# Kernel tuning notes

Hardware: AMD Instinct MI355X
Metric: run time of the kernel (lower is better)

## Reference

```python
import jax, jax.numpy as jnp
import numpy as np

B, N, D = 32, 2048, 128
HALF = D // 2
DT = 0.01  # interval = [0.0, 0.01], euler solver -> single step of size 0.01


def setup_inputs() -> dict:
    key = jax.random.key(0)
    ks = jax.random.split(key, 10)
    x = jax.random.normal(ks[0], (B, N, D), dtype=jnp.float32)
    hz = jax.random.normal(ks[1], (B, N, D), dtype=jnp.float32)
    # row-normalized random adjacency so adj @ h stays O(1) (avoids tanh saturation)
    adj = jax.random.uniform(ks[2], (N, N), dtype=jnp.float32) / N
    W1 = jax.random.normal(ks[3], (D, D), dtype=jnp.float32) * 0.05
    W2 = jax.random.normal(ks[4], (D, D), dtype=jnp.float32) * 0.05
    Wa = jax.random.normal(ks[5], (2 * D, 2 * D), dtype=jnp.float32) * 0.05
    ba = jnp.zeros((2 * D,), dtype=jnp.float32)
    Wb = jax.random.normal(ks[6], (2 * D, D), dtype=jnp.float32) * 0.05
    bb = jnp.zeros((D,), dtype=jnp.float32)
    # nn.Parameter init is zeros in torch; randomize in [0,0.1] for a nontrivial baseline
    eps = jax.random.uniform(ks[7], (B, N, HALF), dtype=jnp.float32) * 0.1
    return {"x": x, "hz": hz, "adj": adj, "W1": W1, "W2": W2,
            "Wa": Wa, "ba": ba, "Wb": Wb, "bb": bb, "eps": eps}


def reference(x, hz, adj, W1, W2, Wa, ba, Wb, bb, eps):
    # MLP gating: Linear(2D,2D) -> ReLU -> Linear(2D,D) -> Tanh
    u = jnp.concatenate([x, hz], axis=-1)            # [B,N,2D]
    h = jnp.tanh(jax.nn.relu(u @ Wa + ba) @ Wb + bb)  # [B,N,D]

    def gnn_func(h, W):
        # f(t, h) = tanh(A @ h @ W)  (graph diffusion ODE func)
        return jnp.tanh(jnp.einsum('nm,bmd->bnd', adj, h) @ W)

    def euler_step(h, W):
        # odeint(euler, t=[0, 0.01]): one step y1 = y0 + dt * f(0, y0)
        return h + DT * gnn_func(h, W)

    eps_c = jnp.clip(eps, 0.0, 0.1)
    for _ in range(2):
        h_f = euler_step(h, W1)[..., :HALF]                      # [B,N,D/2]
        h = jnp.concatenate([h_f, h[..., HALF:]], axis=-1)       # [B,N,D]
        h_s = eps_c * euler_step(h, W2)[..., HALF:]              # [B,N,D/2]
        h = jnp.concatenate([h_f, h_s], axis=-1)                 # [B,N,D]
    return h
```

## Files before the change

### kernel.cpp

```cpp
#include <hip/hip_runtime.h>


typedef unsigned short u16;
typedef unsigned int   u32;
typedef unsigned long long u64;
typedef __attribute__((ext_vector_type(8))) short bf8;
typedef __attribute__((ext_vector_type(4))) float f4;

#define AS1 __attribute__((address_space(1)))
#define AS3 __attribute__((address_space(3)))

__device__ __forceinline__ void gl_lds16(const void* g, void* l) {
  __builtin_amdgcn_global_load_lds((const AS1 u32*)g, (AS3 u32*)l, 16, 0, 0);
}
__device__ __forceinline__ float bf2f(u16 v) {
  u32 u = ((u32)v) << 16; return __builtin_bit_cast(float, u);
}
__device__ __forceinline__ u16 f2bf(float f) {
  u32 u = __builtin_bit_cast(u32, f);
  return (u16)((u + 0x7fffu + ((u >> 16) & 1u)) >> 16);
}
__device__ __forceinline__ float ldf(const void* p, size_t i, u32 isf32) {
  return isf32 ? ((const float*)p)[i] : bf2f(((const u16*)p)[i]);
}

__device__ __forceinline__ void stage128x32(const u16* grow0, int stride, u16* lds,
                                            int wave, int lane) {
  int r0 = wave * 16 + (lane >> 2);
  int c0 = (lane & 3) * 8;
  gl_lds16(grow0 + (size_t)r0 * stride + c0, lds + wave * 512);
  gl_lds16(grow0 + (size_t)(64 + r0) * stride + c0, lds + 2048 + wave * 512);
}

__global__ void detect_dtype(const u16* __restrict__ x_raw, u32* __restrict__ flag) {
  __shared__ int s;
  int tid = threadIdx.x;
  if (tid == 0) s = 0;
  __syncthreads();
  int huge = 0;
#pragma unroll
  for (int j = 0; j < 16; ++j) {
    u16 v = x_raw[tid * 16 + j];
    u32 e = (v >> 7) & 0xFF;
    if (e >= 0xC0) huge = 1;
  }
  if (huge) atomicOr(&s, 1);
  __syncthreads();
  if (tid == 0) flag[0] = (u32)s;
}

__global__ void cvt_bf16(const void* __restrict__ in, u16* __restrict__ out,
                         long in_off, int n, const u32* __restrict__ flag) {
  u32 isf32 = flag[0];
  int gid = blockIdx.x * 256 + threadIdx.x;
  long i = in_off + (long)gid * 4;
  if (gid * 4 >= n) return;
  u16 o0, o1, o2, o3;
  if (isf32) {
    f4 v = *(const f4*)&((const float*)in)[i];
    o0 = f2bf(v[0]); o1 = f2bf(v[1]); o2 = f2bf(v[2]); o3 = f2bf(v[3]);
  } else {
    u64 v = *(const u64*)&((const u16*)in)[i];
    o0 = (u16)v; o1 = (u16)(v >> 16); o2 = (u16)(v >> 32); o3 = (u16)(v >> 48);
  }
  u64 pk = (u64)o0 | ((u64)o1 << 16) | ((u64)o2 << 32) | ((u64)o3 << 48);
  *(u64*)&out[(size_t)gid * 4] = pk;
}

__global__ void prep_weights(const void* __restrict__ Wa, const void* __restrict__ Wb,
                             const void* __restrict__ W1, const void* __restrict__ W2,
                             u16* __restrict__ WaT, u16* __restrict__ WbT,
                             u16* __restrict__ W1T, u16* __restrict__ W2T,
                             const u32* __restrict__ flag) {
  u32 isf32 = flag[0];
  int i = blockIdx.x * 256 + threadIdx.x;
  if (i < 65536) {
    int o = i >> 8, k = i & 255; WaT[o * 256 + k] = f2bf(ldf(Wa, (size_t)k * 256 + o, isf32));
  } else if (i < 98304) {
    int j = i - 65536; int o = j >> 8, k = j & 255;
    WbT[o * 256 + k] = f2bf(ldf(Wb, (size_t)k * 128 + o, isf32));
  } else if (i < 106496) {
    int j = i - 98304; int jj = j >> 7, k = j & 127;
    W1T[jj * 128 + k] = f2bf(ldf(W1, (size_t)k * 128 + jj, isf32));
  } else {
    int j = i - 106496; int jj = j >> 7, k = j & 127;
    W2T[jj * 128 + k] = f2bf(ldf(W2, (size_t)k * 128 + 64 + jj, isf32));
  }
}

__global__ __launch_bounds__(256, 2) void mlp_fused(const void* __restrict__ x,
                                                    const void* __restrict__ hz,
                                                    const u16* __restrict__ WaT,
                                                    const void* __restrict__ ba,
                                                    const u16* __restrict__ WbT,
                                                    const void* __restrict__ bb,
                                                    u16* __restrict__ hT,
                                                    const u32* __restrict__ flag) {
  __shared__ __align__(16) u16 Z[64 * 264];
  __shared__ __align__(16) u16 lA[64 * 32];
  __shared__ __align__(16) u16 lB[256 * 32];
  u32 isf32 = flag[0];
  int tid = threadIdx.x, lane = tid & 63, wave = tid >> 6;
  int col = lane & 15, quad = lane >> 4;
  int r0 = blockIdx.x * 64;

  f4 acc[4][4] = {};
  for (int kk = 0; kk < 8; ++kk) {
    int k0 = kk * 32;
    const void* src = (kk < 4) ? x : hz;
    int csrc = (kk < 4) ? k0 : (k0 - 128);
    __syncthreads();
    {
      int row = tid >> 2, c0 = (tid & 3) * 8;
      size_t g = (size_t)(r0 + row) * 128 + csrc + c0;
      uint4 pk;
      if (isf32) {
        f4 v0 = *(const f4*)&((const float*)src)[g];
        f4 v1 = *(const f4*)&((const float*)src)[g + 4];
        pk.x = (u32)f2bf(v0[0]) | ((u32)f2bf(v0[1]) << 16);
        pk.y = (u32)f2bf(v0[2]) | ((u32)f2bf(v0[3]) << 16);
        pk.z = (u32)f2bf(v1[0]) | ((u32)f2bf(v1[1]) << 16);
        pk.w = (u32)f2bf(v1[2]) | ((u32)f2bf(v1[3]) << 16);
      } else {
        pk = *(const uint4*)&((const u16*)src)[g];
      }
      *(uint4*)&lA[row * 32 + c0] = pk;
    }
    stage128x32(WaT + k0, 256, lB, wave, lane);
    stage128x32(WaT + (size_t)128 * 256 + k0, 256, lB + 4096, wave, lane);
    __syncthreads();
    bf8 af[4], bfr[4];
#pragma unroll
    for (int mi = 0; mi < 4; ++mi) af[mi] = *(const bf8*)&lA[(mi * 16 + col) * 32 + quad * 8];
#pragma unroll
    for (int nj = 0; nj < 4; ++nj) bfr[nj] = *(const bf8*)&lB[(wave * 64 + nj * 16 + col) * 32 + quad * 8];
#pragma unroll
    for (int mi = 0; mi < 4; ++mi)
#pragma unroll
      for (int nj = 0; nj < 4; ++nj)
        acc[mi][nj] = __builtin_amdgcn_mfma_f32_16x16x32_bf16(af[mi], bfr[nj], acc[mi][nj], 0, 0, 0);
  }
#pragma unroll
  for (int mi = 0; mi < 4; ++mi)
#pragma unroll
    for (int nj = 0; nj < 4; ++nj) {
      int o = wave * 64 + nj * 16 + col;
      float bav = ldf(ba, o, isf32);
      int rl = mi * 16 + quad * 4;
#pragma unroll
      for (int r = 0; r < 4; ++r)
        Z[(rl + r) * 264 + o] = f2bf(fmaxf(acc[mi][nj][r] + bav, 0.f));
    }
  __syncthreads();

  f4 acc2[4][2] = {};
  for (int kk = 0; kk < 8; ++kk) {
    int k0 = kk * 32;
    if (kk) __syncthreads();
    stage128x32(WbT + k0, 256, lB, wave, lane);
    __syncthreads();
    bf8 az[4], bw[2];
#pragma unroll
    for (int mi = 0; mi < 4; ++mi) az[mi] = *(const bf8*)&Z[(mi * 16 + col) * 264 + k0 + quad * 8];
#pragma unroll
    for (int nj = 0; nj < 2; ++nj) bw[nj] = *(const bf8*)&lB[(wave * 32 + nj * 16 + col) * 32 + quad * 8];
#pragma unroll
    for (int mi = 0; mi < 4; ++mi)
#pragma unroll
      for (int nj = 0; nj < 2; ++nj)
        acc2[mi][nj] = __builtin_amdgcn_mfma_f32_16x16x32_bf16(az[mi], bw[nj], acc2[mi][nj], 0, 0, 0);
  }
#pragma unroll
  for (int mi = 0; mi < 4; ++mi)
#pragma unroll
    for (int nj = 0; nj < 2; ++nj) {
      int d = wave * 32 + nj * 16 + col;
      float bbv = ldf(bb, d, isf32);
      int rabs = r0 + mi * 16 + quad * 4;
      int b = rabs >> 11, n = rabs & 2047;
      u16 p[4];
#pragma unroll
      for (int r = 0; r < 4; ++r) p[r] = f2bf(tanhf(acc2[mi][nj][r] + bbv));
      u64 pk = (u64)p[0] | ((u64)p[1] << 16) | ((u64)p[2] << 32) | ((u64)p[3] << 48);
      *(u64*)&hT[(size_t)(b * 128 + d) * 2048 + n] = pk;
    }
}

__global__ __launch_bounds__(256, 2) void fused_step(const u16* __restrict__ hin,
                                                     const u16* __restrict__ adjb,
                                                     const u16* __restrict__ WT,
                                                     const void* __restrict__ eps,
                                                     u16* __restrict__ hout,
                                                     int half, const u32* __restrict__ flag) {
  __shared__ __align__(16) u16 lA[2][128 * 32];
  __shared__ __align__(16) u16 lB[2][128 * 32];
  __shared__ __align__(16) u16 gT[128 * 136];
  u32 isf32 = flag[0];
  int tid = threadIdx.x, lane = tid & 63, wave = tid >> 6;
  int wm = wave >> 1, wn = wave & 1, col = lane & 15, quad = lane >> 4;
  int b = blockIdx.y;
  int n0 = blockIdx.x * 128;

  const u16* Arow = hin + (size_t)(b * 128) * 2048;
  const u16* Brow = adjb + (size_t)n0 * 2048;

  stage128x32(Arow, 2048, lA[0], wave, lane);
  stage128x32(Brow, 2048, lB[0], wave, lane);
  __syncthreads();

  f4 acc[4][4] = {};
  for (int kk = 0; kk < 64; ++kk) {
    int cur = kk & 1;
    if (kk < 63) {
      stage128x32(Arow + (kk + 1) * 32, 2048, lA[cur ^ 1], wave, lane);
      stage128x32(Brow + (kk + 1) * 32, 2048, lB[cur ^ 1], wave, lane);
    }
    bf8 af[4], bfr[4];
#pragma unroll
    for (int mi = 0; mi < 4; ++mi) af[mi] = *(const bf8*)&lA[cur][(wm * 64 + mi * 16 + col) * 32 + quad * 8];
#pragma unroll
    for (int nj = 0; nj < 4; ++nj) bfr[nj] = *(const bf8*)&lB[cur][(wn * 64 + nj * 16 + col) * 32 + quad * 8];
#pragma unroll
    for (int mi = 0; mi < 4; ++mi)
#pragma unroll
      for (int nj = 0; nj < 4; ++nj)
        acc[mi][nj] = __builtin_amdgcn_mfma_f32_16x16x32_bf16(af[mi], bfr[nj], acc[mi][nj], 0, 0, 0);
    __syncthreads();
  }
#pragma unroll
  for (int mi = 0; mi < 4; ++mi)
#pragma unroll
    for (int nj = 0; nj < 4; ++nj) {
      int d0 = wm * 64 + mi * 16 + quad * 4;
      int nl = wn * 64 + nj * 16 + col;
      u32 lo = (u32)f2bf(acc[mi][nj][0]) | ((u32)f2bf(acc[mi][nj][1]) << 16);
      u32 hi = (u32)f2bf(acc[mi][nj][2]) | ((u32)f2bf(acc[mi][nj][3]) << 16);
      *(u64*)&gT[nl * 136 + d0] = (u64)lo | ((u64)hi << 32);
    }
  __syncthreads();

  f4 acc2[4][2] = {};
#pragma unroll
  for (int k2 = 0; k2 < 4; ++k2) {
    bf8 aw[4], bg[2];
#pragma unroll
    for (int mi = 0; mi < 4; ++mi)
      aw[mi] = *(const bf8*)&WT[(size_t)(mi * 16 + col) * 128 + k2 * 32 + quad * 8];
#pragma unroll
    for (int nj = 0; nj < 2; ++nj)
      bg[nj] = *(const bf8*)&gT[(wave * 32 + nj * 16 + col) * 136 + k2 * 32 + quad * 8];
#pragma unroll
    for (int mi = 0; mi < 4; ++mi)
#pragma unroll
      for (int nj = 0; nj < 2; ++nj)
        acc2[mi][nj] = __builtin_amdgcn_mfma_f32_16x16x32_bf16(aw[mi], bg[nj], acc2[mi][nj], 0, 0, 0);
  }

  bool has_eps = (eps != nullptr);
#pragma unroll
  for (int mi = 0; mi < 4; ++mi)
#pragma unroll
    for (int nj = 0; nj < 2; ++nj) {
      int j0 = mi * 16 + quad * 4;
      int nl = wave * 32 + nj * 16 + col;
      int n = n0 + nl;
      float ev[4];
      if (has_eps) {
        size_t eoff = ((size_t)b * 2048 + n) * 64 + j0;
        if (isf32) {
          f4 e = *(const f4*)&((const float*)eps)[eoff];
          ev[0] = e[0]; ev[1] = e[1]; ev[2] = e[2]; ev[3] = e[3];
        } else {
          u64 e = *(const u64*)&((const u16*)eps)[eoff];
          ev[0] = bf2f((u16)e); ev[1] = bf2f((u16)(e >> 16));
          ev[2] = bf2f((u16)(e >> 32)); ev[3] = bf2f((u16)(e >> 48));
        }
      }
#pragma unroll
      for (int r = 0; r < 4; ++r) {
        int j = j0 + r;
        size_t idx = (size_t)(b * 128 + half * 64 + j) * 2048 + n;
        float hold = bf2f(hin[idx]);
        float nh = hold + 0.01f * tanhf(acc2[mi][nj][r]);
        if (has_eps) {
          float e = fminf(fmaxf(ev[r], 0.f), 0.1f);
          nh = e * nh;
        }
        hout[idx] = f2bf(nh);
      }
    }

  {
    int oh = (1 - half) * 64;
    const u16* src = hin + (size_t)(b * 128 + oh) * 2048 + n0;
    u16* dst = hout + (size_t)(b * 128 + oh) * 2048 + n0;
#pragma unroll
    for (int i = 0; i < 4; ++i) {
      int idx = i * 256 + tid;
      int rr = idx >> 4;
      int cc = (idx & 15) * 8;
      *(uint4*)&dst[(size_t)rr * 2048 + cc] = *(const uint4*)&src[(size_t)rr * 2048 + cc];
    }
  }
}

__global__ void untranspose(const u16* __restrict__ hT, void* __restrict__ out,
                            const u32* __restrict__ flag) {
  __shared__ __align__(16) u16 t[64][65];
  u32 isf32 = flag[0];
  int b = blockIdx.z, d0 = blockIdx.y * 64, n0 = blockIdx.x * 64;
  int tid = threadIdx.x;
#pragma unroll
  for (int i = 0; i < 16; ++i) {
    int idx = tid + i * 256;
    int r = idx >> 6, c = idx & 63;
    t[r][c] = hT[(size_t)(b * 128 + d0 + r) * 2048 + n0 + c];
  }
  __syncthreads();
#pragma unroll
  for (int i = 0; i < 16; ++i) {
    int idx = tid + i * 256;
    int r = idx >> 6, c = idx & 63;
    size_t o = (size_t)(b * 2048 + n0 + r) * 128 + d0 + c;
    if (isf32) ((float*)out)[o] = bf2f(t[c][r]);
    else       ((u16*)out)[o] = t[c][r];
  }
}

extern "C" void kernel_launch(void* const* d_in, const int* in_sizes, int n_in,
                              void* d_out, int out_size, void* d_ws, size_t ws_size,
                              hipStream_t stream) {
  const void* x   = d_in[0];
  const void* hz  = d_in[1];
  const void* adj = d_in[2];
  const void* W1  = d_in[3];
  const void* W2  = d_in[4];
  const void* Wa  = d_in[5];
  const void* ba  = d_in[6];
  const void* Wb  = d_in[7];
  const void* bb  = d_in[8];
  const void* eps = d_in[9];

  char* ws = (char*)d_ws;
  u16* hA   = (u16*)(ws);
  u16* adjb = (u16*)(ws + (17ull << 20));
  u16* WaT  = (u16*)(ws + (26ull << 20));
  u16* WbT  = WaT + 256 * 256;
  u16* W1T  = WbT + 128 * 256;
  u16* W2T  = W1T + 64 * 128;
  u32* flag = (u32*)(W2T + 64 * 128);
  u16* hB   = (u16*)d_out;

  detect_dtype<<<dim3(1), dim3(256), 0, stream>>>((const u16*)x, flag);
  prep_weights<<<dim3(448), dim3(256), 0, stream>>>(Wa, Wb, W1, W2, WaT, WbT, W1T, W2T, flag);
  cvt_bf16<<<dim3(4096), dim3(256), 0, stream>>>(adj, adjb, 0, 4194304, flag);
  mlp_fused<<<dim3(1024), dim3(256), 0, stream>>>(x, hz, WaT, ba, WbT, bb, hA, flag);
  fused_step<<<dim3(16, 32), dim3(256), 0, stream>>>(hA, adjb, W1T, nullptr, hB, 0, flag);
  fused_step<<<dim3(16, 32), dim3(256), 0, stream>>>(hB, adjb, W2T, eps, hA, 1, flag);
  fused_step<<<dim3(16, 32), dim3(256), 0, stream>>>(hA, adjb, W1T, nullptr, hB, 0, flag);
  fused_step<<<dim3(16, 32), dim3(256), 0, stream>>>(hB, adjb, W2T, eps, hA, 1, flag);
  untranspose<<<dim3(32, 2, 32), dim3(256), 0, stream>>>(hA, d_out, flag);
}
```

Baseline: 412.1 us.

## Reassociate adj@(h@W) so graph GEMM contracts only 64 needed columns

Uses associativity to compute h@W (only the 64 output columns each step needs) before the adjacency product. The projection is fused into the epilogue of the previous kernel (MLP or prior step), which writes a transposed hW buffer. The big N×N GEMM then has a 64-wide rather than 128-wide operand, halving its MFMA work and A-operand traffic. In exchange, the main loop now stages 4 K-slices per barrier without double buffering, and extra bf16 rounding of the intermediate hW alters numerics.

```diff
diff --git a/kernel.cpp b/kernel.cpp
--- a/kernel.cpp
+++ b/kernel.cpp
@@ -30,6 +30,11 @@
   int c0 = (lane & 3) * 8;
   gl_lds16(grow0 + (size_t)r0 * stride + c0, lds + wave * 512);
   gl_lds16(grow0 + (size_t)(64 + r0) * stride + c0, lds + 2048 + wave * 512);
+}
+__device__ __forceinline__ void stage64x32(const u16* grow0, int stride, u16* lds,
+                                           int wave, int lane) {
+  gl_lds16(grow0 + (size_t)(wave * 16 + (lane >> 2)) * stride + (lane & 3) * 8,
+           lds + wave * 512);
 }
 
 __global__ void detect_dtype(const u16* __restrict__ x_raw, u32* __restrict__ flag) {
@@ -94,15 +99,20 @@
                                                     const void* __restrict__ ba,
                                                     const u16* __restrict__ WbT,
                                                     const void* __restrict__ bb,
+                                                    const u16* __restrict__ W1T,
                                                     u16* __restrict__ hT,
+                                                    u16* __restrict__ hW,
                                                     const u32* __restrict__ flag) {
   __shared__ __align__(16) u16 Z[64 * 264];
-  __shared__ __align__(16) u16 lA[64 * 32];
-  __shared__ __align__(16) u16 lB[256 * 32];
+  __shared__ __align__(16) u16 pool[10240];
+  u16* lA = pool;
+  u16* lB = pool + 2048;
+  u16* hN = pool;
   u32 isf32 = flag[0];
   int tid = threadIdx.x, lane = tid & 63, wave = tid >> 6;
   int col = lane & 15, quad = lane >> 4;
   int r0 = blockIdx.x * 64;
+  int b = r0 >> 11;
 
   f4 acc[4][4] = {};
   for (int kk = 0; kk < 8; ++kk) {
@@ -170,93 +180,101 @@
       for (int nj = 0; nj < 2; ++nj)
         acc2[mi][nj] = __builtin_amdgcn_mfma_f32_16x16x32_bf16(az[mi], bw[nj], acc2[mi][nj], 0, 0, 0);
   }
+  __syncthreads();
+
 #pragma unroll
   for (int mi = 0; mi < 4; ++mi)
 #pragma unroll
     for (int nj = 0; nj < 2; ++nj) {
       int d = wave * 32 + nj * 16 + col;
       float bbv = ldf(bb, d, isf32);
-      int rabs = r0 + mi * 16 + quad * 4;
-      int b = rabs >> 11, n = rabs & 2047;
+      int rl = mi * 16 + quad * 4;
+      int rabs = r0 + rl;
+      int n = rabs & 2047;
       u16 p[4];
 #pragma unroll
-      for (int r = 0; r < 4; ++r) p[r] = f2bf(tanhf(acc2[mi][nj][r] + bbv));
+      for (int r = 0; r < 4; ++r) {
+        p[r] = f2bf(tanhf(acc2[mi][nj][r] + bbv));
+        hN[(rl + r) * 136 + d] = p[r];
+      }
       u64 pk = (u64)p[0] | ((u64)p[1] << 16) | ((u64)p[2] << 32) | ((u64)p[3] << 48);
       *(u64*)&hT[(size_t)(b * 128 + d) * 2048 + n] = pk;
     }
-}
-
-__global__ __launch_bounds__(256, 2) void fused_step(const u16* __restrict__ hin,
-                                                     const u16* __restrict__ adjb,
-                                                     const u16* __restrict__ WT,
-                                                     const void* __restrict__ eps,
-                                                     u16* __restrict__ hout,
-                                                     int half, const u32* __restrict__ flag) {
-  __shared__ __align__(16) u16 lA[2][128 * 32];
-  __shared__ __align__(16) u16 lB[2][128 * 32];
-  __shared__ __align__(16) u16 gT[128 * 136];
+  __syncthreads();
+
+  f4 acc3[4] = {};
+#pragma unroll
+  for (int ks = 0; ks < 4; ++ks) {
+    bf8 aw[4], bg;
+#pragma unroll
+    for (int mi = 0; mi < 4; ++mi)
+      aw[mi] = *(const bf8*)&W1T[(size_t)(mi * 16 + col) * 128 + ks * 32 + quad * 8];
+    bg = *(const bf8*)&hN[(wave * 16 + col) * 136 + ks * 32 + quad * 8];
+#pragma unroll
+    for (int mi = 0; mi < 4; ++mi)
+      acc3[mi] = __builtin_amdgcn_mfma_f32_16x16x32_bf16(aw[mi], bg, acc3[mi], 0, 0, 0);
+  }
+#pragma unroll
+  for (int mi = 0; mi < 4; ++mi) {
+    int rloc = wave * 16 + col;
+    int ng = (r0 & 2047) + rloc;
+#pragma unroll
+    for (int r = 0; r < 4; ++r) {
+      int j = mi * 16 + quad * 4 + r;
+      hW[(size_t)(b * 64 + j) * 2048 + ng] = f2bf(acc3[mi][r]);
+    }
+  }
+}
+
+__global__ __launch_bounds__(256, 2) void fused_step2(const u16* __restrict__ hin,
+                                                      const u16* __restrict__ hWT,
+                                                      const u16* __restrict__ adjb,
+                                                      const u16* __restrict__ WnT,
+                                                      const void* __restrict__ eps,
+                                                      u16* __restrict__ hout,
+                                                      u16* __restrict__ hWout,
+                                                      int half, const u32* __restrict__ flag) {
+  __shared__ __align__(16) u16 smem[24576];
+  u16* lA = smem;
+  u16* lB = smem + 8192;
+  u16* gN = smem;
   u32 isf32 = flag[0];
   int tid = threadIdx.x, lane = tid & 63, wave = tid >> 6;
-  int wm = wave >> 1, wn = wave & 1, col = lane & 15, quad = lane >> 4;
+  int col = lane & 15, quad = lane >> 4;
   int b = blockIdx.y;
   int n0 = blockIdx.x * 128;
 
-  const u16* Arow = hin + (size_t)(b * 128) * 2048;
+  const u16* Arow = hWT + (size_t)(b * 64) * 2048;
   const u16* Brow = adjb + (size_t)n0 * 2048;
 
-  stage128x32(Arow, 2048, lA[0], wave, lane);
-  stage128x32(Brow, 2048, lB[0], wave, lane);
-  __syncthreads();
-
-  f4 acc[4][4] = {};
-  for (int kk = 0; kk < 64; ++kk) {
-    int cur = kk & 1;
-    if (kk < 63) {
-      stage128x32(Arow + (kk + 1) * 32, 2048, lA[cur ^ 1], wave, lane);
-      stage128x32(Brow + (kk + 1) * 32, 2048, lB[cur ^ 1], wave, lane);
-    }
-    bf8 af[4], bfr[4];
-#pragma unroll
-    for (int mi = 0; mi < 4; ++mi) af[mi] = *(const bf8*)&lA[cur][(wm * 64 + mi * 16 + col) * 32 + quad * 8];
-#pragma unroll
-    for (int nj = 0; nj < 4; ++nj) bfr[nj] = *(const bf8*)&lB[cur][(wn * 64 + nj * 16 + col) * 32 + quad * 8];
-#pragma unroll
-    for (int mi = 0; mi < 4; ++mi)
-#pragma unroll
-      for (int nj = 0; nj < 4; ++nj)
-        acc[mi][nj] = __builtin_amdgcn_mfma_f32_16x16x32_bf16(af[mi], bfr[nj], acc[mi][nj], 0, 0, 0);
-    __syncthreads();
-  }
-#pragma unroll
-  for (int mi = 0; mi < 4; ++mi)
-#pragma unroll
-    for (int nj = 0; nj < 4; ++nj) {
-      int d0 = wm * 64 + mi * 16 + quad * 4;
-      int nl = wn * 64 + nj * 16 + col;
-      u32 lo = (u32)f2bf(acc[mi][nj][0]) | ((u32)f2bf(acc[mi][nj][1]) << 16);
-      u32 hi = (u32)f2bf(acc[mi][nj][2]) | ((u32)f2bf(acc[mi][nj][3]) << 16);
-      *(u64*)&gT[nl * 136 + d0] = (u64)lo | ((u64)hi << 32);
-    }
-  __syncthreads();
-
-  f4 acc2[4][2] = {};
-#pragma unroll
-  for (int k2 = 0; k2 < 4; ++k2) {
-    bf8 aw[4], bg[2];
-#pragma unroll
-    for (int mi = 0; mi < 4; ++mi)
-      aw[mi] = *(const bf8*)&WT[(size_t)(mi * 16 + col) * 128 + k2 * 32 + quad * 8];
-#pragma unroll
-    for (int nj = 0; nj < 2; ++nj)
-      bg[nj] = *(const bf8*)&gT[(wave * 32 + nj * 16 + col) * 136 + k2 * 32 + quad * 8];
-#pragma unroll
-    for (int mi = 0; mi < 4; ++mi)
-#pragma unroll
-      for (int nj = 0; nj < 2; ++nj)
-        acc2[mi][nj] = __builtin_amdgcn_mfma_f32_16x16x32_bf16(aw[mi], bg[nj], acc2[mi][nj], 0, 0, 0);
+  f4 acc[4][2] = {};
+  for (int kk = 0; kk < 16; ++kk) {
+    int k0 = kk * 128;
+#pragma unroll
+    for (int p = 0; p < 4; ++p) {
+      stage64x32(Arow + k0 + p * 32, 2048, lA + p * 2048, wave, lane);
+      stage128x32(Brow + k0 + p * 32, 2048, lB + p * 4096, wave, lane);
+    }
+    __syncthreads();
+#pragma unroll
+    for (int p = 0; p < 4; ++p) {
+      bf8 af[4], bfr[2];
+#pragma unroll
+      for (int mi = 0; mi < 4; ++mi) af[mi] = *(const bf8*)&lA[p * 2048 + (mi * 16 + col) * 32 + quad * 8];
+#pragma unroll
+      for (int nj = 0; nj < 2; ++nj) bfr[nj] = *(const bf8*)&lB[p * 4096 + (wave * 32 + nj * 16 + col) * 32 + quad * 8];
+#pragma unroll
+      for (int mi = 0; mi < 4; ++mi)
+#pragma unroll
+        for (int nj = 0; nj < 2; ++nj)
+          acc[mi][nj] = __builtin_amdgcn_mfma_f32_16x16x32_bf16(af[mi], bfr[nj], acc[mi][nj], 0, 0, 0);
+    }
+    __syncthreads();
   }
 
   bool has_eps = (eps != nullptr);
+  bool mk_hw = (WnT != nullptr);
+  int dBase = half * 64;
 #pragma unroll
   for (int mi = 0; mi < 4; ++mi)
 #pragma unroll
@@ -276,17 +294,23 @@
           ev[2] = bf2f((u16)(e >> 32)); ev[3] = bf2f((u16)(e >> 48));
         }
       }
+      u16 pv[4];
 #pragma unroll
       for (int r = 0; r < 4; ++r) {
         int j = j0 + r;
-        size_t idx = (size_t)(b * 128 + half * 64 + j) * 2048 + n;
+        size_t idx = (size_t)(b * 128 + dBase + j) * 2048 + n;
         float hold = bf2f(hin[idx]);
-        float nh = hold + 0.01f * tanhf(acc2[mi][nj][r]);
+        float nh = hold + 0.01f * tanhf(acc[mi][nj][r]);
         if (has_eps) {
           float e = fminf(fmaxf(ev[r], 0.f), 0.1f);
           nh = e * nh;
         }
-        hout[idx] = f2bf(nh);
+        pv[r] = f2bf(nh);
+        hout[idx] = pv[r];
+      }
+      if (mk_hw) {
+        u64 pk = (u64)pv[0] | ((u64)pv[1] << 16) | ((u64)pv[2] << 32) | ((u64)pv[3] << 48);
+        *(u64*)&gN[nl * 136 + dBase + j0] = pk;
       }
     }
 
@@ -299,8 +323,45 @@
       int idx = i * 256 + tid;
       int rr = idx >> 4;
       int cc = (idx & 15) * 8;
-      *(uint4*)&dst[(size_t)rr * 2048 + cc] = *(const uint4*)&src[(size_t)rr * 2048 + cc];
-    }
+      uint4 v = *(const uint4*)&src[(size_t)rr * 2048 + cc];
+      *(uint4*)&dst[(size_t)rr * 2048 + cc] = v;
+      if (mk_hw) {
+        u16 t[8];
+        *(uint4*)t = v;
+#pragma unroll
+        for (int q = 0; q < 8; ++q) gN[(cc + q) * 136 + oh + rr] = t[q];
+      }
+    }
+  }
+
+  if (mk_hw) {
+    __syncthreads();
+    f4 acc2[4][2] = {};
+#pragma unroll
+    for (int ks = 0; ks < 4; ++ks) {
+      bf8 aw[4], bg[2];
+#pragma unroll
+      for (int mi = 0; mi < 4; ++mi)
+        aw[mi] = *(const bf8*)&WnT[(size_t)(mi * 16 + col) * 128 + ks * 32 + quad * 8];
+#pragma unroll
+      for (int nj = 0; nj < 2; ++nj)
+        bg[nj] = *(const bf8*)&gN[(wave * 32 + nj * 16 + col) * 136 + ks * 32 + quad * 8];
+#pragma unroll
+      for (int mi = 0; mi < 4; ++mi)
+#pragma unroll
+        for (int nj = 0; nj < 2; ++nj)
+          acc2[mi][nj] = __builtin_amdgcn_mfma_f32_16x16x32_bf16(aw[mi], bg[nj], acc2[mi][nj], 0, 0, 0);
+    }
+#pragma unroll
+    for (int mi = 0; mi < 4; ++mi)
+#pragma unroll
+      for (int nj = 0; nj < 2; ++nj) {
+        int jp0 = mi * 16 + quad * 4;
+        int n = n0 + wave * 32 + nj * 16 + col;
+#pragma unroll
+        for (int r = 0; r < 4; ++r)
+          hWout[(size_t)(b * 64 + jp0 + r) * 2048 + n] = f2bf(acc2[mi][nj][r]);
+      }
   }
 }
 
@@ -344,7 +405,9 @@
   char* ws = (char*)d_ws;
   u16* hA   = (u16*)(ws);
   u16* adjb = (u16*)(ws + (17ull << 20));
-  u16* WaT  = (u16*)(ws + (26ull << 20));
+  u16* hWa  = (u16*)(ws + (26ull << 20));
+  u16* hWb  = (u16*)(ws + (35ull << 20));
+  u16* WaT  = (u16*)(ws + (44ull << 20));
   u16* WbT  = WaT + 256 * 256;
   u16* W1T  = WbT + 128 * 256;
   u16* W2T  = W1T + 64 * 128;
@@ -354,10 +417,10 @@
   detect_dtype<<<dim3(1), dim3(256), 0, stream>>>((const u16*)x, flag);
   prep_weights<<<dim3(448), dim3(256), 0, stream>>>(Wa, Wb, W1, W2, WaT, WbT, W1T, W2T, flag);
   cvt_bf16<<<dim3(4096), dim3(256), 0, stream>>>(adj, adjb, 0, 4194304, flag);
-  mlp_fused<<<dim3(1024), dim3(256), 0, stream>>>(x, hz, WaT, ba, WbT, bb, hA, flag);
-  fused_step<<<dim3(16, 32), dim3(256), 0, stream>>>(hA, adjb, W1T, nullptr, hB, 0, flag);
-  fused_step<<<dim3(16, 32), dim3(256), 0, stream>>>(hB, adjb, W2T, eps, hA, 1, flag);
-  fused_step<<<dim3(16, 32), dim3(256), 0, stream>>>(hA, adjb, W1T, nullptr, hB, 0, flag);
-  fused_step<<<dim3(16, 32), dim3(256), 0, stream>>>(hB, adjb, W2T, eps, hA, 1, flag);
+  mlp_fused<<<dim3(1024), dim3(256), 0, stream>>>(x, hz, WaT, ba, WbT, bb, W1T, hA, hWa, flag);
+  fused_step2<<<dim3(16, 32), dim3(256), 0, stream>>>(hA, hWa, adjb, W2T, nullptr, hB, hWb, 0, flag);
+  fused_step2<<<dim3(16, 32), dim3(256), 0, stream>>>(hB, hWb, adjb, W1T, eps, hA, hWa, 1, flag);
+  fused_step2<<<dim3(16, 32), dim3(256), 0, stream>>>(hA, hWa, adjb, W2T, nullptr, hB, hWb, 0, flag);
+  fused_step2<<<dim3(16, 32), dim3(256), 0, stream>>>(hB, hWb, adjb, nullptr, eps, hA, nullptr, 1, flag);
   untranspose<<<dim3(32, 2, 32), dim3(256), 0, stream>>>(hA, d_out, flag);
 }
```

Measured after the change: 350.1 us. 15.1% less time.
